# Kernel optimization log

Measured on AMD Instinct MI355X. Metric: run time of the kernel, lower is better.

The kernel has to match this reference:

```python
import jax, jax.numpy as jnp
import numpy as np

B, N, D = 1, 40962, 512
H, HD = 4, 128            # num_heads, key_size=value_size=d_model//num_heads
BS = 256                  # mask_block_size
NB = 161                  # num blocks = ceil(N/BS)
NP = NB * BS              # padded nodes = 41216
PAD = NP - N              # num_padding_nodes = 254
C = 16                    # global_norm_conditioning dim
FFW = 4 * D
SCALE = HD ** -0.5


def _build_mask():
    valid = (np.arange(NP) < N).reshape(NB, BS)            # key validity per block
    md = np.broadcast_to(valid[:, None, :], (NB, BS, BS))  # diag: keys of block n
    mu = np.zeros((NB, BS, BS), bool)
    mu[:-1] = np.broadcast_to(valid[1:, None, :], (NB - 1, BS, BS))   # upper: block n+1
    ml = np.zeros((NB, BS, BS), bool)
    ml[1:] = np.broadcast_to(valid[:-1, None, :], (NB - 1, BS, BS))   # lower: block n-1
    m = np.stack([md, mu, ml])[None, :, :, None]           # [1,3,NB,1,BS,BS]
    return jnp.asarray(m)


def setup_inputs() -> dict:
    key = jax.random.key(0)
    ks = jax.random.split(key, 12)
    s = 0.02
    return {
        'x': jax.random.normal(ks[0], (B, N, D), jnp.float32),
        'global_norm_conditioning': jax.random.normal(ks[1], (B, C), jnp.float32),
        'mask': _build_mask(),
        'wq': jax.random.normal(ks[2], (D, H * HD), jnp.float32) * s,
        'wk': jax.random.normal(ks[3], (D, H * HD), jnp.float32) * s,
        'wv': jax.random.normal(ks[4], (D, H * HD), jnp.float32) * s,
        'w_final': jax.random.normal(ks[5], (H * HD, D), jnp.float32) * s,
        'b_final': jnp.zeros((D,), jnp.float32),
        'w_up': jax.random.normal(ks[6], (D, FFW), jnp.float32) * s,
        'b_up': jnp.zeros((FFW,), jnp.float32),
        'w_down': jax.random.normal(ks[7], (FFW, D), jnp.float32) * s,
        'b_down': jnp.zeros((D,), jnp.float32),
        'w_cond': jax.random.normal(ks[8], (C, 2 * D), jnp.float32) * s,
        'b_cond': jnp.zeros((2 * D,), jnp.float32),
    }


def _layernorm(h):
    mu = h.mean(-1, keepdims=True)
    var = h.var(-1, keepdims=True)
    return (h - mu) * jax.lax.rsqrt(var + 1e-5)


def _triblock_attn(h, mask, wq, wk, wv, w_final, b_final):
    hp = jnp.pad(h, ((0, 0), (0, PAD), (0, 0))).reshape(B, NB, BS, D)
    q = (hp @ wq).reshape(B, NB, BS, H, HD)
    k = (hp @ wk).reshape(B, NB, BS, H, HD)
    v = (hp @ wv).reshape(B, NB, BS, H, HD)
    k = jnp.pad(k, ((0, 0), (1, 1), (0, 0), (0, 0), (0, 0)))
    v = jnp.pad(v, ((0, 0), (1, 1), (0, 0), (0, 0), (0, 0)))
    qk = lambda kk: jnp.einsum('bnqhd,bnkhd->bnhqk', q, kk) * SCALE
    ld = jnp.where(mask[:, 0], qk(k[:, 1:-1]), -1e30)
    lu = jnp.where(mask[:, 1], qk(k[:, 2:]), -1e30)
    ll = jnp.where(mask[:, 2], qk(k[:, :-2]), -1e30)
    # tri-block softmax with shared max/denominator
    m = jnp.maximum(jnp.maximum(
        jax.lax.stop_gradient(ld.max(-1, keepdims=True)),
        jax.lax.stop_gradient(lu.max(-1, keepdims=True))),
        jax.lax.stop_gradient(ll.max(-1, keepdims=True)))
    ed, eu, el = jnp.exp(ld - m), jnp.exp(lu - m), jnp.exp(ll - m)
    denom = ed.sum(-1, keepdims=True) + eu.sum(-1, keepdims=True) + el.sum(-1, keepdims=True)
    av = lambda w, vv: jnp.einsum('bnhqk,bnkhd->bnqhd', w, vv)
    o = av(ed / denom, v[:, 1:-1]) + av(eu / denom, v[:, 2:]) + av(el / denom, v[:, :-2])
    o = o.reshape(B, NP, H * HD) @ w_final + b_final
    return o[:, :N, :]


def reference(x, global_norm_conditioning, mask, wq, wk, wv, w_final, b_final,
              w_up, b_up, w_down, b_down, w_cond, b_cond):
    so = global_norm_conditioning @ w_cond + b_cond       # [B, 2D]
    scale, offset = jnp.split(so[:, None, :], 2, axis=-1)  # [B,1,D] each
    cond = lambda h: h * (scale + 1.0) + offset
    x = x + _triblock_attn(cond(_layernorm(x)), mask, wq, wk, wv, w_final, b_final)
    h = cond(_layernorm(x))
    x = x + (jax.nn.gelu(h @ w_up + b_up) @ w_down + b_down)
    return x
```

## Files before the change

kernel.cpp:

```cpp
#include <hip/hip_runtime.h>
#include <stdint.h>
#include <stddef.h>

#define NNODES 40962
#define NBLK   161
#define NP     41216
#define DM     512
#define NH     4
#define HD     128
#define SCALE_ATT 0.08838834764831845f

typedef __attribute__((ext_vector_type(8))) short short8;
typedef __attribute__((ext_vector_type(4))) float f32x4;
typedef __attribute__((ext_vector_type(4))) unsigned short us4;
typedef __attribute__((ext_vector_type(2))) unsigned long long u64x2;
typedef __attribute__((ext_vector_type(8))) __bf16 bf16x8;

__device__ __forceinline__ unsigned short f2bf(float f){
  unsigned u = __builtin_bit_cast(unsigned, f);
  u += 0x7fffu + ((u >> 16) & 1u);
  return (unsigned short)(u >> 16);
}
__device__ __forceinline__ float bf2f(unsigned short h){
  unsigned u = ((unsigned)h) << 16;
  return __builtin_bit_cast(float, u);
}
__device__ __forceinline__ unsigned char f2fp8(float f){
  return (unsigned char)(__builtin_amdgcn_cvt_pk_fp8_f32(f, 0.f, 0, false) & 0xff);
}
__device__ __forceinline__ float gelu_tanh(float x){
  float y = 0.7978845608028654f * (x + 0.044715f * x * x * x);
  y = fminf(fmaxf(y, -15.f), 15.f);
  float t = __expf(2.f * y);
  return x * t / (t + 1.f);
}
#define MFMA8(a,b,c) __builtin_amdgcn_mfma_f32_16x16x32_fp8_fp8((a),(b),(c),0,0,0)

#define GLOAD16(g, l) \
  __builtin_amdgcn_global_load_lds((const __attribute__((address_space(1))) unsigned int*)(g), \
                                   (__attribute__((address_space(3))) unsigned int*)(l), 16, 0, 0)

__global__ void k_cond(const float* __restrict__ gnc, const float* __restrict__ wc,
                       const float* __restrict__ bc, float* __restrict__ cond){
  int j = blockIdx.x * 256 + threadIdx.x;
  float acc = bc[j];
  #pragma unroll
  for(int c = 0; c < 16; ++c) acc += gnc[c] * wc[c * 1024 + j];
  cond[j] = (j < 512) ? acc + 1.0f : acc;
}

__global__ __launch_bounds__(256) void k_transpose_f8(const float* __restrict__ W,
                                                      unsigned char* __restrict__ Wt,
                                                      int K, int Ncols){
  __shared__ float tile[32][33];
  int n0 = blockIdx.x * 32, k0 = blockIdx.y * 32;
  int tx = threadIdx.x & 31, ty = threadIdx.x >> 5;
  #pragma unroll
  for(int i = 0; i < 4; ++i){
    int r = ty + i * 8;
    tile[r][tx] = W[(size_t)(k0 + r) * Ncols + n0 + tx];
  }
  __syncthreads();
  #pragma unroll
  for(int i = 0; i < 4; ++i){
    int r = ty + i * 8;
    Wt[(size_t)(n0 + r) * K + k0 + tx] = f2fp8(tile[tx][r]);
  }
}

__global__ __launch_bounds__(256) void k_lncond(const void* __restrict__ xin, int in_bf16,
                                                const float* __restrict__ cond,
                                                void* __restrict__ outv, int out_f8,
                                                int Mvalid){
  int lane = threadIdx.x & 63;
  int row = blockIdx.x * 4 + (threadIdx.x >> 6);
  if(row >= Mvalid){
    if(out_f8){
      unsigned char* orow = (unsigned char*)outv + (size_t)row * DM + lane * 8;
      *(uint2*)orow = make_uint2(0, 0);
    } else {
      unsigned short* orow = (unsigned short*)outv + (size_t)row * DM + lane * 8;
      *(uint4*)orow = make_uint4(0,0,0,0);
    }
    return;
  }
  float v[8];
  if(in_bf16){
    const unsigned short* xr = (const unsigned short*)xin + (size_t)row * DM + lane * 8;
    us4 a = *(const us4*)xr, b = *(const us4*)(xr + 4);
    #pragma unroll
    for(int j = 0; j < 4; ++j){ v[j] = bf2f(a[j]); v[4+j] = bf2f(b[j]); }
  } else {
    const float* xr = (const float*)xin + (size_t)row * DM + lane * 8;
    float4 a = *(const float4*)xr;
    float4 b = *(const float4*)(xr + 4);
    v[0]=a.x; v[1]=a.y; v[2]=a.z; v[3]=a.w; v[4]=b.x; v[5]=b.y; v[6]=b.z; v[7]=b.w;
  }
  float s = 0.f, s2 = 0.f;
  #pragma unroll
  for(int j = 0; j < 8; ++j){ s += v[j]; s2 += v[j]*v[j]; }
  #pragma unroll
  for(int off = 1; off < 64; off <<= 1){ s += __shfl_xor(s, off); s2 += __shfl_xor(s2, off); }
  float mu = s * (1.f/DM);
  float var = s2 * (1.f/DM) - mu*mu;
  float rs = rsqrtf(var + 1e-5f);
  float scv[8], ofv[8];
  {
    float4 sc0 = *(const float4*)(cond + lane*8);
    float4 sc1 = *(const float4*)(cond + lane*8 + 4);
    float4 of0 = *(const float4*)(cond + 512 + lane*8);
    float4 of1 = *(const float4*)(cond + 512 + lane*8 + 4);
    scv[0]=sc0.x;scv[1]=sc0.y;scv[2]=sc0.z;scv[3]=sc0.w;
    scv[4]=sc1.x;scv[5]=sc1.y;scv[6]=sc1.z;scv[7]=sc1.w;
    ofv[0]=of0.x;ofv[1]=of0.y;ofv[2]=of0.z;ofv[3]=of0.w;
    ofv[4]=of1.x;ofv[5]=of1.y;ofv[6]=of1.z;ofv[7]=of1.w;
  }
  float o8[8];
  #pragma unroll
  for(int j = 0; j < 8; ++j) o8[j] = (v[j] - mu) * rs * scv[j] + ofv[j];
  if(out_f8){
    unsigned char* orow = (unsigned char*)outv + (size_t)row * DM + lane * 8;
    unsigned lo = 0, hi = 0;
    #pragma unroll
    for(int j = 0; j < 4; ++j) lo |= ((unsigned)f2fp8(o8[j])) << (8*j);
    #pragma unroll
    for(int j = 0; j < 4; ++j) hi |= ((unsigned)f2fp8(o8[4+j])) << (8*j);
    *(uint2*)orow = make_uint2(lo, hi);
  } else {
    unsigned short* orow = (unsigned short*)outv + (size_t)row * DM + lane * 8;
    unsigned pk[4];
    #pragma unroll
    for(int j = 0; j < 4; ++j)
      pk[j] = (unsigned)f2bf(o8[2*j]) | ((unsigned)f2bf(o8[2*j+1]) << 16);
    *(uint4*)orow = make_uint4(pk[0],pk[1],pk[2],pk[3]);
  }
}

#define GF_GELU   1
#define GF_RESF32 4
#define GF_QKV    8
#define GF_F8OUT  16

__global__ __launch_bounds__(256, 3)
void k_g128_f8(const unsigned char* __restrict__ A, int lda,
               const unsigned char* __restrict__ Bt, int ldb,
               const float* __restrict__ bias,
               const void* __restrict__ resid, int ldr,
               void* __restrict__ out, int ldo,
               void* __restrict__ out_k, void* __restrict__ out_vt,
               int Mstore, int NT, int Nblks, int flags)
{
  __shared__ __align__(16) unsigned char As[128*128];
  __shared__ __align__(16) unsigned char Bs[128*128];
  const int tid = threadIdx.x;
  const int lane = tid & 63, l15 = lane & 15, lg = lane >> 4;
  const int w = tid >> 6, wm = w >> 1, wn = w & 1;
  int nwg = gridDim.x;
  int q = nwg >> 3, r = nwg & 7;
  int xcd = blockIdx.x & 7, idx = blockIdx.x >> 3;
  int sid = (xcd < r ? xcd * (q + 1) : r * (q + 1) + (xcd - r) * q) + idx;
  int mblk = sid / Nblks, nblk = sid % Nblks;
  const int m0 = mblk * 128, n0 = nblk * 128;

  int srow[4], scol[4];
  #pragma unroll
  for(int rr = 0; rr < 4; ++rr){
    unsigned L = (unsigned)rr * 4096u + (unsigned)tid * 16u;
    unsigned sw = L ^ (((L >> 7) & 7u) << 4);
    srow[rr] = sw >> 7;
    scol[rr] = sw & 127u;
  }
  const unsigned wbase = (unsigned)w * 1024u;

  f32x4 acc[4][4];
  #pragma unroll
  for(int i = 0; i < 4; ++i)
    #pragma unroll
    for(int j = 0; j < 4; ++j) acc[i][j] = (f32x4)0.0f;

  for(int ks = 0; ks < NT; ++ks){
    #pragma unroll
    for(int rr = 0; rr < 4; ++rr)
      GLOAD16(A + (size_t)(m0 + srow[rr]) * lda + ks*128 + scol[rr],
              (char*)As + rr*4096 + wbase);
    #pragma unroll
    for(int rr = 0; rr < 4; ++rr)
      GLOAD16(Bt + (size_t)(n0 + srow[rr]) * ldb + ks*128 + scol[rr],
              (char*)Bs + rr*4096 + wbase);
    __syncthreads();
    #pragma unroll
    for(int kk = 0; kk < 4; ++kk){
      const unsigned csw = (unsigned)((kk*32 + lg*8) ^ ((l15 & 7) << 4));
      long la[4], lb[4];
      #pragma unroll
      for(int mi = 0; mi < 4; ++mi)
        la[mi] = *(const long*)(As + (wm*64 + mi*16 + l15)*128 + csw);
      #pragma unroll
      for(int ni = 0; ni < 4; ++ni)
        lb[ni] = *(const long*)(Bs + (wn*64 + ni*16 + l15)*128 + csw);
      #pragma unroll
      for(int mi = 0; mi < 4; ++mi)
        #pragma unroll
        for(int ni = 0; ni < 4; ++ni)
          acc[mi][ni] = MFMA8(la[mi], lb[ni], acc[mi][ni]);
    }
    __syncthreads();
  }

  #pragma unroll
  for(int mi = 0; mi < 4; ++mi){
    int rowb = m0 + wm*64 + mi*16 + lg*4;
    #pragma unroll
    for(int ni = 0; ni < 4; ++ni){
      int col = n0 + wn*64 + ni*16 + l15;
      float bc = bias ? bias[col] : 0.f;
      float vv[4];
      #pragma unroll
      for(int rr = 0; rr < 4; ++rr){
        float tt = acc[mi][ni][rr] + bc;
        if(flags & GF_GELU) tt = gelu_tanh(tt);
        vv[rr] = tt;
      }
      if(flags & GF_QKV){
        if(n0 < 512){
          #pragma unroll
          for(int rr = 0; rr < 4; ++rr)
            ((unsigned char*)out)[(size_t)(rowb + rr)*ldo + col] = f2fp8(vv[rr]);
        } else if(n0 < 1024){
          #pragma unroll
          for(int rr = 0; rr < 4; ++rr)
            ((unsigned char*)out_k)[(size_t)(rowb + rr)*ldo + col - 512] = f2fp8(vv[rr]);
        } else {
          unsigned pk = 0;
          #pragma unroll
          for(int rr = 0; rr < 4; ++rr) pk |= ((unsigned)f2fp8(vv[rr])) << (8*rr);
          *(unsigned*)((unsigned char*)out_vt + (size_t)(col - 1024)*NP + rowb) = pk;
        }
      } else if(flags & GF_F8OUT){
        #pragma unroll
        for(int rr = 0; rr < 4; ++rr)
          ((unsigned char*)out)[(size_t)(rowb + rr)*ldo + col] = f2fp8(vv[rr]);
      } else if(flags & GF_RESF32){
        #pragma unroll
        for(int rr = 0; rr < 4; ++rr){
          int row = rowb + rr;
          if(row < Mstore){
            float tt = vv[rr] + ((const float*)resid)[(size_t)row*ldr + col];
            ((unsigned short*)out)[(size_t)row*ldo + col] = f2bf(tt);
          }
        }
      } else {
        #pragma unroll
        for(int rr = 0; rr < 4; ++rr){
          int row = rowb + rr;
          if(row < Mstore){
            float tt = vv[rr]
                     + bf2f(((const unsigned short*)resid)[(size_t)row*ldr + col]);
            ((float*)out)[(size_t)row*ldo + col] = tt;
          }
        }
      }
    }
  }
}

__global__ __launch_bounds__(512, 4)
void k_attn(const unsigned char* __restrict__ q_g, const unsigned char* __restrict__ k_g,
            const unsigned char* __restrict__ vt_g, unsigned char* __restrict__ o_g8)
{
  __shared__ __align__(16) unsigned char kv[128*128];
  __shared__ __align__(16) unsigned char p_lds[8*16*136];
  int b = blockIdx.x;
  int g = (b & 7) * 161 + (b >> 3);
  int n = g >> 3, rg = (g >> 2) & 1, h = g & 3;
  int tid = threadIdx.x;
  int w = tid >> 6, lane = tid & 63, l15 = lane & 15, lg = lane >> 4;
  int qbase = n*256 + rg*128 + w*16;
  unsigned char* pw = p_lds + w*16*136;
  const int rsw = l15 << 3;
  const int srow = tid >> 3, scs = (tid & 7) * 16;

  long aq[4];
  {
    const unsigned char* qp = q_g + (size_t)(qbase + l15)*DM + h*HD;
    #pragma unroll
    for(int kb = 0; kb < 4; ++kb) aq[kb] = *(const long*)(qp + kb*32 + lg*8);
  }
  f32x4 oacc[8];
  #pragma unroll
  for(int t = 0; t < 8; ++t) oacc[t] = (f32x4)0.0f;
  float denom[4] = {0.f,0.f,0.f,0.f};

  #define COORDS(j, K0, VCH) do {                                    \
    int d_ = (j) >> 1, ch_ = (j) & 1;                                \
    int nb_ = n + (d_ == 1 ? 1 : (d_ == 2 ? -1 : 0));                \
    int nbc_ = nb_ < 0 ? 0 : (nb_ >= NBLK ? NBLK - 1 : nb_);         \
    (K0) = nbc_*256 + ch_*128;                                       \
    (VCH) = (nb_ >= 0) && (nb_ < NBLK) && ((K0) < NNODES);           \
  } while(0)

  u64x2 kreg[2], vreg[2];
  int k0; bool vch;
  COORDS(0, k0, vch);
  #pragma unroll
  for(int i = 0; i < 2; ++i){
    int row = srow + i*64;
    kreg[i] = *(const u64x2*)(k_g + (size_t)(k0+row)*DM + h*HD + scs);
    vreg[i] = *(const u64x2*)(vt_g + (size_t)(h*HD+row)*NP + k0 + scs);
  }

  #pragma unroll 1
  for(int j = 0; j < 6; ++j){
    int k0n = 0; bool vchn = false;
    const bool hn = (j < 5);
    if(hn) COORDS(j+1, k0n, vchn);
    __syncthreads();
    #pragma unroll
    for(int i = 0; i < 2; ++i){
      int row = srow + i*64;
      int base = row*128, sz = (row & 15) << 3;
      *(unsigned long long*)(kv + base + ((scs    ) ^ sz)) = kreg[i][0];
      *(unsigned long long*)(kv + base + ((scs + 8) ^ sz)) = kreg[i][1];
    }
    __syncthreads();
    if(hn){
      #pragma unroll
      for(int i = 0; i < 2; ++i){
        int row = srow + i*64;
        kreg[i] = *(const u64x2*)(k_g + (size_t)(k0n+row)*DM + h*HD + scs);
      }
    }
    float rsum[4] = {0.f,0.f,0.f,0.f};
    #pragma unroll
    for(int t = 0; t < 8; ++t){
      f32x4 s = (f32x4)0.0f;
      #pragma unroll
      for(int kb = 0; kb < 4; ++kb){
        long bk = *(const long*)(kv + (t*16 + l15)*128 + ((kb*32 + lg*8) ^ rsw));
        s = MFMA8(aq[kb], bk, s);
      }
      bool kval = vch && ((k0 + t*16 + l15) < NNODES);
      #pragma unroll
      for(int r = 0; r < 4; ++r){
        float p = kval ? __expf(s[r] * SCALE_ATT) : 0.f;
        rsum[r] += p;
        pw[(lg*4 + r)*136 + t*16 + l15] = f2fp8(p);
      }
    }
    #pragma unroll
    for(int r = 0; r < 4; ++r){
      float s_ = rsum[r];
      s_ += __shfl_xor(s_, 1); s_ += __shfl_xor(s_, 2);
      s_ += __shfl_xor(s_, 4); s_ += __shfl_xor(s_, 8);
      denom[r] += s_;
    }
    __syncthreads();
    #pragma unroll
    for(int i = 0; i < 2; ++i){
      int row = srow + i*64;
      int base = row*128, sz = (row & 15) << 3;
      *(unsigned long long*)(kv + base + ((scs    ) ^ sz)) = vreg[i][0];
      *(unsigned long long*)(kv + base + ((scs + 8) ^ sz)) = vreg[i][1];
    }
    __syncthreads();
    if(hn){
      #pragma unroll
      for(int i = 0; i < 2; ++i){
        int row = srow + i*64;
        vreg[i] = *(const u64x2*)(vt_g + (size_t)(h*HD+row)*NP + k0n + scs);
      }
    }
    __builtin_amdgcn_s_setprio(1);
    #pragma unroll
    for(int kb2 = 0; kb2 < 4; ++kb2){
      long ap = *(const long*)(pw + l15*136 + kb2*32 + lg*8);
      #pragma unroll
      for(int t2 = 0; t2 < 8; ++t2){
        long bv = *(const long*)(kv + (t2*16 + l15)*128 + ((kb2*32 + lg*8) ^ rsw));
        oacc[t2] = MFMA8(ap, bv, oacc[t2]);
      }
    }
    __builtin_amdgcn_s_setprio(0);
    k0 = k0n; vch = vchn;
  }
  float inv[4];
  #pragma unroll
  for(int r = 0; r < 4; ++r) inv[r] = 1.0f / denom[r];
  #pragma unroll
  for(int t2 = 0; t2 < 8; ++t2){
    #pragma unroll
    for(int r = 0; r < 4; ++r){
      o_g8[(size_t)(qbase + lg*4 + r)*DM + h*HD + t2*16 + l15] =
        f2fp8(oacc[t2][r] * inv[r]);
    }
  }
}

extern "C" void kernel_launch(void* const* d_in, const int* in_sizes, int n_in,
                              void* d_out, int out_size, void* d_ws, size_t ws_size,
                              hipStream_t stream)
{
  const float* x    = (const float*)d_in[0];
  const float* gnc  = (const float*)d_in[1];
  const float* wq   = (const float*)d_in[3];
  const float* wk   = (const float*)d_in[4];
  const float* wv   = (const float*)d_in[5];
  const float* wf   = (const float*)d_in[6];
  const float* bfin = (const float*)d_in[7];
  const float* wup  = (const float*)d_in[8];
  const float* bup  = (const float*)d_in[9];
  const float* wdn  = (const float*)d_in[10];
  const float* bdn  = (const float*)d_in[11];
  const float* wc   = (const float*)d_in[12];
  const float* bc   = (const float*)d_in[13];
  float* out = (float*)d_out;

  char* ws = (char*)d_ws;
  size_t off = 0;
  auto alloc = [&](size_t bytes)->void*{
    void* p = ws + off;
    off += (bytes + 255) & ~(size_t)255;
    return p;
  };
  float*          cond    = (float*)alloc(1024u*4);
  unsigned char*  wqkv_f8 = (unsigned char*)alloc((size_t)1536*512);
  unsigned char*  wf_f8   = (unsigned char*)alloc((size_t)512*512);
  unsigned char*  wup_f8  = (unsigned char*)alloc((size_t)2048*512);
  unsigned char*  wdn_f8  = (unsigned char*)alloc((size_t)512*2048);
  unsigned char*  hp8     = (unsigned char*)alloc((size_t)NP*DM);
  unsigned char*  kbuf8   = (unsigned char*)alloc((size_t)NP*DM);
  unsigned char*  vtbuf8  = (unsigned char*)alloc((size_t)NP*DM);
  unsigned char*  qbuf8   = (unsigned char*)alloc((size_t)NP*DM);
  unsigned char*  obuf8   = (unsigned char*)alloc((size_t)NP*DM);
  unsigned short* x1      = (unsigned short*)alloc((size_t)NP*DM*2);
  unsigned char*  ubuf8   = (unsigned char*)alloc((size_t)NP*2048);
  (void)ws_size; (void)in_sizes; (void)n_in; (void)out_size;

  k_cond<<<4, 256, 0, stream>>>(gnc, wc, bc, cond);
  k_transpose_f8<<<dim3(16,16), 256, 0, stream>>>(wq, wqkv_f8,            512, 512);
  k_transpose_f8<<<dim3(16,16), 256, 0, stream>>>(wk, wqkv_f8 + 512*512,  512, 512);
  k_transpose_f8<<<dim3(16,16), 256, 0, stream>>>(wv, wqkv_f8 + 1024*512, 512, 512);
  k_transpose_f8<<<dim3(16,16), 256, 0, stream>>>(wf, wf_f8,  512, 512);
  k_transpose_f8<<<dim3(64,16), 256, 0, stream>>>(wup, wup_f8, 512, 2048);
  k_transpose_f8<<<dim3(16,64), 256, 0, stream>>>(wdn, wdn_f8, 2048, 512);
  k_lncond<<<NP/4, 256, 0, stream>>>(x, 0, cond, hp8, 1, NNODES);
  k_g128_f8<<<322*12, 256, 0, stream>>>(hp8, 512, wqkv_f8, 512, nullptr, nullptr, 0,
                                        qbuf8, 512, kbuf8, vtbuf8, NP, 4, 12, GF_QKV);
  k_attn<<<1288, 512, 0, stream>>>(qbuf8, kbuf8, vtbuf8, obuf8);
  k_g128_f8<<<322*4, 256, 0, stream>>>(obuf8, 512, wf_f8, 512, bfin, x, 512,
                                       x1, 512, nullptr, nullptr, NNODES, 4, 4,
                                       GF_RESF32);
  k_lncond<<<NP/4, 256, 0, stream>>>(x1, 1, cond, hp8, 1, NNODES);
  k_g128_f8<<<322*16, 256, 0, stream>>>(hp8, 512, wup_f8, 512, bup, nullptr, 0,
                                        ubuf8, 2048, nullptr, nullptr, NP, 4, 16,
                                        GF_GELU | GF_F8OUT);
  k_g128_f8<<<322*4, 256, 0, stream>>>(ubuf8, 2048, wdn_f8, 2048, bdn, x1, 512,
                                       out, 512, nullptr, nullptr, NNODES, 16, 4, 0);
}
```

Before: 514.9 us.

## Permute fp8 K-dimension layout so GEMM loads 16-byte LDS vectors

Introduces a column permutation within each 128-byte K chunk, applied consistently to transposed weights, LayerNorm fp8 outputs, fp8 GEMM outputs and attention outputs. The GEMM inner loop can then fetch all four k-substeps per lane with two 16-byte LDS reads instead of four 8-byte reads, cutting LDS instruction count. The permutation is applied identically to both operands, so the dot products are unchanged. It touches several producers and raises register pressure for the preloaded fragments.

```diff
diff --git a/kernel.cpp b/kernel.cpp
--- a/kernel.cpp
+++ b/kernel.cpp
@@ -14,7 +14,6 @@
 typedef __attribute__((ext_vector_type(4))) float f32x4;
 typedef __attribute__((ext_vector_type(4))) unsigned short us4;
 typedef __attribute__((ext_vector_type(2))) unsigned long long u64x2;
-typedef __attribute__((ext_vector_type(8))) __bf16 bf16x8;
 
 __device__ __forceinline__ unsigned short f2bf(float f){
   unsigned u = __builtin_bit_cast(unsigned, f);
@@ -27,6 +26,9 @@
 }
 __device__ __forceinline__ unsigned char f2fp8(float f){
   return (unsigned char)(__builtin_amdgcn_cvt_pk_fp8_f32(f, 0.f, 0, false) & 0xff);
+}
+__device__ __forceinline__ int permc(int c){
+  return (c & ~0x78) | ((c & 0x60) >> 2) | ((c & 0x18) << 2);
 }
 __device__ __forceinline__ float gelu_tanh(float x){
   float y = 0.7978845608028654f * (x + 0.044715f * x * x * x);
@@ -64,7 +66,8 @@
   #pragma unroll
   for(int i = 0; i < 4; ++i){
     int r = ty + i * 8;
-    Wt[(size_t)(n0 + r) * K + k0 + tx] = f2fp8(tile[tx][r]);
+    int k = k0 + tx;
+    Wt[(size_t)(n0 + r) * K + permc(k)] = f2fp8(tile[tx][r]);
   }
 }
 
@@ -76,8 +79,8 @@
   int row = blockIdx.x * 4 + (threadIdx.x >> 6);
   if(row >= Mvalid){
     if(out_f8){
-      unsigned char* orow = (unsigned char*)outv + (size_t)row * DM + lane * 8;
-      *(uint2*)orow = make_uint2(0, 0);
+      unsigned char* orow = (unsigned char*)outv + (size_t)row * DM + permc(lane * 8);
+      *(unsigned long long*)orow = 0ull;
     } else {
       unsigned short* orow = (unsigned short*)outv + (size_t)row * DM + lane * 8;
       *(uint4*)orow = make_uint4(0,0,0,0);
@@ -119,13 +122,13 @@
   #pragma unroll
   for(int j = 0; j < 8; ++j) o8[j] = (v[j] - mu) * rs * scv[j] + ofv[j];
   if(out_f8){
-    unsigned char* orow = (unsigned char*)outv + (size_t)row * DM + lane * 8;
+    unsigned char* orow = (unsigned char*)outv + (size_t)row * DM + permc(lane * 8);
     unsigned lo = 0, hi = 0;
     #pragma unroll
     for(int j = 0; j < 4; ++j) lo |= ((unsigned)f2fp8(o8[j])) << (8*j);
     #pragma unroll
     for(int j = 0; j < 4; ++j) hi |= ((unsigned)f2fp8(o8[4+j])) << (8*j);
-    *(uint2*)orow = make_uint2(lo, hi);
+    *(unsigned long long*)orow = ((unsigned long long)hi << 32) | lo;
   } else {
     unsigned short* orow = (unsigned short*)outv + (size_t)row * DM + lane * 8;
     unsigned pk[4];
@@ -188,22 +191,27 @@
       GLOAD16(Bt + (size_t)(n0 + srow[rr]) * ldb + ks*128 + scol[rr],
               (char*)Bs + rr*4096 + wbase);
     __syncthreads();
-    #pragma unroll
-    for(int kk = 0; kk < 4; ++kk){
-      const unsigned csw = (unsigned)((kk*32 + lg*8) ^ ((l15 & 7) << 4));
-      long la[4], lb[4];
-      #pragma unroll
-      for(int mi = 0; mi < 4; ++mi)
-        la[mi] = *(const long*)(As + (wm*64 + mi*16 + l15)*128 + csw);
-      #pragma unroll
-      for(int ni = 0; ni < 4; ++ni)
-        lb[ni] = *(const long*)(Bs + (wn*64 + ni*16 + l15)*128 + csw);
+    u64x2 la[4][2], lb[4][2];
+    #pragma unroll
+    for(int mi = 0; mi < 4; ++mi)
+      #pragma unroll
+      for(int p = 0; p < 2; ++p)
+        la[mi][p] = *(const u64x2*)(As + (wm*64 + mi*16 + l15)*128 +
+                                    ((lg*32 + p*16) ^ ((l15 & 7) << 4)));
+    #pragma unroll
+    for(int ni = 0; ni < 4; ++ni)
+      #pragma unroll
+      for(int p = 0; p < 2; ++p)
+        lb[ni][p] = *(const u64x2*)(Bs + (wn*64 + ni*16 + l15)*128 +
+                                    ((lg*32 + p*16) ^ ((l15 & 7) << 4)));
+    #pragma unroll
+    for(int kk = 0; kk < 4; ++kk)
       #pragma unroll
       for(int mi = 0; mi < 4; ++mi)
         #pragma unroll
         for(int ni = 0; ni < 4; ++ni)
-          acc[mi][ni] = MFMA8(la[mi], lb[ni], acc[mi][ni]);
-    }
+          acc[mi][ni] = MFMA8((long)la[mi][kk>>1][kk&1],
+                              (long)lb[ni][kk>>1][kk&1], acc[mi][ni]);
     __syncthreads();
   }
 
@@ -237,9 +245,10 @@
           *(unsigned*)((unsigned char*)out_vt + (size_t)(col - 1024)*NP + rowb) = pk;
         }
       } else if(flags & GF_F8OUT){
+        int pc = permc(col);
         #pragma unroll
         for(int rr = 0; rr < 4; ++rr)
-          ((unsigned char*)out)[(size_t)(rowb + rr)*ldo + col] = f2fp8(vv[rr]);
+          ((unsigned char*)out)[(size_t)(rowb + rr)*ldo + pc] = f2fp8(vv[rr]);
       } else if(flags & GF_RESF32){
         #pragma unroll
         for(int rr = 0; rr < 4; ++rr){
@@ -388,10 +397,10 @@
   for(int r = 0; r < 4; ++r) inv[r] = 1.0f / denom[r];
   #pragma unroll
   for(int t2 = 0; t2 < 8; ++t2){
+    int pc = permc(h*HD + t2*16 + l15);
     #pragma unroll
     for(int r = 0; r < 4; ++r){
-      o_g8[(size_t)(qbase + lg*4 + r)*DM + h*HD + t2*16 + l15] =
-        f2fp8(oacc[t2][r] * inv[r]);
+      o_g8[(size_t)(qbase + lg*4 + r)*DM + pc] = f2fp8(oacc[t2][r] * inv[r]);
     }
   }
 }
```

Measured after the change: 507.4 us (median of 2 runs). Within noise of the previous version (-1.5%).
